# Performance work log

Measured on AMD Instinct MI355X. Metric: run time of the kernel, lower is better.

The kernel has to match this reference:

```python
import jax, jax.numpy as jnp
import numpy as np

EMBED_DIM = 768
FF_MULT = 4
HIDDEN = EMBED_DIM * FF_MULT
BATCH, SEQ = 32, 1024
EPS = 1e-6


def rmsnorm(x, g):
    # RMSNorm over last dim with learned scale g
    return x * jax.lax.rsqrt(jnp.mean(x * x, axis=-1, keepdims=True) + EPS) * g


def act_quant(x):
    # per-token int8 absmax quantization (BitNet b1.58)
    scale = 127.0 / jnp.clip(jnp.max(jnp.abs(x), axis=-1, keepdims=True), 1e-5, None)
    return jnp.clip(jnp.round(x * scale), -128.0, 127.0) / scale


def weight_quant(w):
    # per-tensor ternary (1.58-bit) absmean quantization
    scale = 1.0 / jnp.clip(jnp.mean(jnp.abs(w)), 1e-5, None)
    return jnp.clip(jnp.round(w * scale), -1.0, 1.0) / scale


def bitlinear(x, w, g):
    xn = rmsnorm(x, g)
    # straight-through estimator: forward uses quantized values
    xq = xn + jax.lax.stop_gradient(act_quant(xn) - xn)
    wq = w + jax.lax.stop_gradient(weight_quant(w) - w)
    return jnp.einsum('bsd,fd->bsf', xq, wq)


def setup_inputs() -> dict:
    key = jax.random.key(0)
    k1, k2, k3 = jax.random.split(key, 3)
    x = jax.random.normal(k1, (BATCH, SEQ, EMBED_DIM), dtype=jnp.float32)
    w1 = jax.random.normal(k2, (HIDDEN, EMBED_DIM), dtype=jnp.float32) * 0.02
    w2 = jax.random.normal(k3, (EMBED_DIM, HIDDEN), dtype=jnp.float32) * 0.02
    g1 = jnp.ones((EMBED_DIM,), dtype=jnp.float32)
    g2 = jnp.ones((HIDDEN,), dtype=jnp.float32)
    return {"x": x, "w1": w1, "g1": g1, "w2": w2, "g2": g2}


def reference(x, w1, g1, w2, g2):
    # BitFeedForward: BitLinear -> GELU (exact, matches nn.GELU) -> BitLinear
    # Dropout(p=0.0) is identity.
    h = jax.nn.gelu(bitlinear(x, w1, g1), approximate=False)
    return bitlinear(h, w2, g2)
```

## Files before the change

### kernel.cpp

```cpp
#include <hip/hip_runtime.h>
#include <hip/hip_bf16.h>
#include <hip/hip_fp16.h>
#include <math.h>

#define TOKENS 32768
#define EMBED  768
#define HIDDEN 3072
#define WELEMS (EMBED*HIDDEN)

typedef __attribute__((ext_vector_type(4))) int i32x4;
typedef signed char i8;

__device__ __forceinline__ float wave_reduce_sum(float v) {
    for (int o = 32; o > 0; o >>= 1) v += __shfl_down(v, o);
    return v;
}
__device__ __forceinline__ float wave_reduce_max(float v) {
    for (int o = 32; o > 0; o >>= 1) v = fmaxf(v, __shfl_down(v, o));
    return v;
}

__device__ __forceinline__ float gelu_tanh(float x) {
    const float x2 = x * x;
    const float u  = 0.7978845608f * x * fmaf(0.044715f, x2, 1.0f);
    const float ex = __expf(u + u);
    const float r  = __builtin_amdgcn_rcpf(ex + 1.0f);
    const float th = fmaf(-2.0f, r, 1.0f);
    const float hx = 0.5f * x;
    return fmaf(hx, th, hx);
}

__device__ __forceinline__ unsigned int q8pack4(float v0, float v1, float v2,
                                                float v3, float qs) {
    union { float f; unsigned int i; } u0, u1, u2, u3;
    u0.f = fmaf(v0, qs, 12582912.0f);
    u1.f = fmaf(v1, qs, 12582912.0f);
    u2.f = fmaf(v2, qs, 12582912.0f);
    u3.f = fmaf(v3, qs, 12582912.0f);
    return (u0.i & 0xFFu) | ((u1.i & 0xFFu) << 8) |
           ((u2.i & 0xFFu) << 16) | ((u3.i & 0xFFu) << 24);
}

__global__ __launch_bounds__(256) void k_abs_partial(const float* __restrict__ w,
                                                     float* __restrict__ out, int n) {
    float s = 0.f;
    for (int i = blockIdx.x * 256 + threadIdx.x; i < n; i += gridDim.x * 256)
        s += fabsf(w[i]);
    __shared__ float red[4];
    s = wave_reduce_sum(s);
    if ((threadIdx.x & 63) == 0) red[threadIdx.x >> 6] = s;
    __syncthreads();
    if (threadIdx.x == 0) out[blockIdx.x] = red[0] + red[1] + red[2] + red[3];
}

__global__ __launch_bounds__(256) void k_finalize(const float* __restrict__ p,
                                                  float* __restrict__ m) {
    __shared__ float r1[4], r2[4];
    float s1 = 0.f, s2 = 0.f;
    for (int i = threadIdx.x; i < 512; i += 256) { s1 += p[i]; s2 += p[512 + i]; }
    s1 = wave_reduce_sum(s1); s2 = wave_reduce_sum(s2);
    if ((threadIdx.x & 63) == 0) { r1[threadIdx.x >> 6] = s1; r2[threadIdx.x >> 6] = s2; }
    __syncthreads();
    if (threadIdx.x == 0) {
        float m1 = (r1[0] + r1[1] + r1[2] + r1[3]) / (float)WELEMS;
        float m2 = (r2[0] + r2[1] + r2[2] + r2[3]) / (float)WELEMS;
        m[0] = fmaxf(m1, 1e-5f);
        m[1] = fmaxf(m2, 1e-5f);
    }
}

__global__ __launch_bounds__(256) void k_quant_w(const float* __restrict__ w,
                                                 i8* __restrict__ wq,
                                                 const float* __restrict__ mp, int n) {
    const float inv = 1.0f / mp[0];
    for (int i = blockIdx.x * 256 + threadIdx.x; i < n; i += gridDim.x * 256) {
        float q = rintf(w[i] * inv);
        q = fminf(1.f, fmaxf(-1.f, q));
        wq[i] = (i8)(int)q;
    }
}

template <int D>
__global__ __launch_bounds__(256) void k_rms_quant_f32(const float* __restrict__ x,
                                                       const float* __restrict__ g,
                                                       i8* __restrict__ xq,
                                                       float* __restrict__ sc) {
    constexpr int NV = D / 4;
    constexpr int IT = (NV + 255) / 256;
    __shared__ float reds[4], redm[4];
    const int t = blockIdx.x;
    const float4* xp = reinterpret_cast<const float4*>(x + (size_t)t * D);
    const float4* gp = reinterpret_cast<const float4*>(g);
    float4 xg[IT];
    float ssq = 0.f, amax = 0.f;
#pragma unroll
    for (int i = 0; i < IT; ++i) {
        const int idx = i * 256 + (int)threadIdx.x;
        const bool act = (NV % 256 == 0) || (idx < NV);
        if (act) {
            float4 v = xp[idx];
            float4 gv = gp[idx];
            ssq += v.x * v.x + v.y * v.y + v.z * v.z + v.w * v.w;
            xg[i].x = v.x * gv.x; xg[i].y = v.y * gv.y;
            xg[i].z = v.z * gv.z; xg[i].w = v.w * gv.w;
            amax = fmaxf(amax, fmaxf(fmaxf(fabsf(xg[i].x), fabsf(xg[i].y)),
                                     fmaxf(fabsf(xg[i].z), fabsf(xg[i].w))));
        } else {
            xg[i].x = xg[i].y = xg[i].z = xg[i].w = 0.f;
        }
    }
    ssq = wave_reduce_sum(ssq);
    amax = wave_reduce_max(amax);
    if ((threadIdx.x & 63) == 0) { reds[threadIdx.x >> 6] = ssq; redm[threadIdx.x >> 6] = amax; }
    __syncthreads();
    const float S = reds[0] + reds[1] + reds[2] + reds[3];
    const float A = fmaxf(fmaxf(redm[0], redm[1]), fmaxf(redm[2], redm[3]));
    const float rs = (float)(1.0 / sqrt((double)S / D + 1e-6));
    const float an = fmaxf(A * rs, 1e-5f);
    const float qs = rs * (127.0f / an);
    if (threadIdx.x == 0) sc[t] = an * (1.0f / 127.0f);
    unsigned int* op = reinterpret_cast<unsigned int*>(xq + (size_t)t * D);
#pragma unroll
    for (int i = 0; i < IT; ++i) {
        const int idx = i * 256 + (int)threadIdx.x;
        const bool act = (NV % 256 == 0) || (idx < NV);
        if (act)
            op[idx] = q8pack4(xg[i].x, xg[i].y, xg[i].z, xg[i].w, qs);
    }
}

template <int D>
__global__ __launch_bounds__(256) void k_rms_quant_f16(const __half* __restrict__ x,
                                                       const float* __restrict__ g,
                                                       i8* __restrict__ xq,
                                                       float* __restrict__ sc) {
    constexpr int NV = D / 8;
    constexpr int IT = (NV + 255) / 256;
    __shared__ float reds[4], redm[4];
    const int t = blockIdx.x;
    const int4* xp = reinterpret_cast<const int4*>(x + (size_t)t * D);
    const float4* gp = reinterpret_cast<const float4*>(g);
    float xg[IT][8];
    float ssq = 0.f, amax = 0.f;
#pragma unroll
    for (int i = 0; i < IT; ++i) {
        const int idx = i * 256 + (int)threadIdx.x;
        const bool act = (NV % 256 == 0) || (idx < NV);
        if (act) {
            int4 raw = xp[idx];
            const __half2* hp = reinterpret_cast<const __half2*>(&raw);
            float4 g0 = gp[idx * 2];
            float4 g1 = gp[idx * 2 + 1];
            float gv[8] = {g0.x, g0.y, g0.z, g0.w, g1.x, g1.y, g1.z, g1.w};
#pragma unroll
            for (int j = 0; j < 4; ++j) {
                float2 f = __half22float2(hp[j]);
                float a0 = f.x, a1 = f.y;
                ssq += a0 * a0 + a1 * a1;
                xg[i][j * 2]     = a0 * gv[j * 2];
                xg[i][j * 2 + 1] = a1 * gv[j * 2 + 1];
                amax = fmaxf(amax, fmaxf(fabsf(xg[i][j * 2]), fabsf(xg[i][j * 2 + 1])));
            }
        } else {
#pragma unroll
            for (int j = 0; j < 8; ++j) xg[i][j] = 0.f;
        }
    }
    ssq = wave_reduce_sum(ssq);
    amax = wave_reduce_max(amax);
    if ((threadIdx.x & 63) == 0) { reds[threadIdx.x >> 6] = ssq; redm[threadIdx.x >> 6] = amax; }
    __syncthreads();
    const float S = reds[0] + reds[1] + reds[2] + reds[3];
    const float A = fmaxf(fmaxf(redm[0], redm[1]), fmaxf(redm[2], redm[3]));
    const float rs = (float)(1.0 / sqrt((double)S / D + 1e-6));
    const float an = fmaxf(A * rs, 1e-5f);
    const float qs = rs * (127.0f / an);
    if (threadIdx.x == 0) sc[t] = an * (1.0f / 127.0f);
    unsigned int* op = reinterpret_cast<unsigned int*>(xq + (size_t)t * D);
#pragma unroll
    for (int i = 0; i < IT; ++i) {
        const int idx = i * 256 + (int)threadIdx.x;
        const bool act = (NV % 256 == 0) || (idx < NV);
        if (act) {
            op[idx * 2]     = q8pack4(xg[i][0], xg[i][1], xg[i][2], xg[i][3], qs);
            op[idx * 2 + 1] = q8pack4(xg[i][4], xg[i][5], xg[i][6], xg[i][7], qs);
        }
    }
}

template <int BN, bool GELU, typename OutT>
__global__ __launch_bounds__(512, 4)
void k_gemm_i8(const i8* __restrict__ A, const i8* __restrict__ B,
               OutT* __restrict__ C, const float* __restrict__ rsc,
               const float* __restrict__ msc, int nbx, int N, int K) {
    constexpr int NI = BN / 64;
    __shared__ i8 As[128 * 128];
    __shared__ i8 Bs[BN * 128];

    const int nwg = (int)gridDim.x;
    const int id  = (int)blockIdx.x;
    const int q = nwg >> 3, r = nwg & 7;
    const int xcd = id & 7, sub = id >> 3;
    const int swz = (xcd < r ? xcd * (q + 1) : r * (q + 1) + (xcd - r) * q) + sub;
    const int bx = swz % nbx;
    const int by = swz / nbx;

    const int tid  = (int)threadIdx.x;
    const int lane = tid & 63;
    const int wave = tid >> 6;
    const int wr = wave >> 2, wc = wave & 3;
    const size_t rowBase = (size_t)by * 128;
    const size_t colBase = (size_t)bx * BN;
    const float ms = msc[0];

    i32x4 acc[4][NI] = {};

    const int srow = tid >> 3;
    const int cc   = tid & 7;
    const int gcol = (cc ^ (srow & 7)) * 16;
    const i8* gA0 = A + (rowBase + srow) * (size_t)K + gcol;
    const i8* gB0 = B + (colBase + srow) * (size_t)K + gcol;
    const int lOff = srow * 128 + cc * 16;

    const int frow = lane & 15;
    const int fko  = (lane >> 4) * 16;
    const int rswz = (frow & 7) << 4;

    for (int k0 = 0; k0 < K; k0 += 128) {
#pragma unroll
        for (int r2 = 0; r2 < 2; ++r2)
            __builtin_amdgcn_global_load_lds(
                (const __attribute__((address_space(1))) void*)(gA0 + (size_t)r2 * 64 * K + k0),
                (__attribute__((address_space(3))) void*)(&As[lOff + r2 * 64 * 128]), 16, 0, 0);
#pragma unroll
        for (int r4 = 0; r4 < BN / 64; ++r4)
            __builtin_amdgcn_global_load_lds(
                (const __attribute__((address_space(1))) void*)(gB0 + (size_t)r4 * 64 * K + k0),
                (__attribute__((address_space(3))) void*)(&Bs[lOff + r4 * 64 * 128]), 16, 0, 0);
        __syncthreads();
#pragma unroll
        for (int ks = 0; ks < 2; ++ks) {
            i32x4 af[4], bv[NI];
#pragma unroll
            for (int mi = 0; mi < 4; ++mi)
                af[mi] = *(const i32x4*)(&As[(wr * 64 + mi * 16 + frow) * 128
                                             + ((ks * 64 + fko) ^ rswz)]);
#pragma unroll
            for (int ni = 0; ni < NI; ++ni)
                bv[ni] = *(const i32x4*)(&Bs[(wc * (BN / 4) + ni * 16 + frow) * 128
                                             + ((ks * 64 + fko) ^ rswz)]);
#pragma unroll
            for (int mi = 0; mi < 4; ++mi)
#pragma unroll
                for (int ni = 0; ni < NI; ++ni)
                    acc[mi][ni] = __builtin_amdgcn_mfma_i32_16x16x64_i8(
                        af[mi], bv[ni], acc[mi][ni], 0, 0, 0);
        }
        __syncthreads();
    }

    const int ccol = lane & 15;
    const int crg  = lane >> 4;
#pragma unroll
    for (int mi = 0; mi < 4; ++mi) {
#pragma unroll
        for (int i = 0; i < 4; ++i) {
            size_t row = rowBase + wr * 64 + mi * 16 + crg * 4 + i;
            float rscale = rsc[row] * ms;
#pragma unroll
            for (int ni = 0; ni < NI; ++ni) {
                size_t col = colBase + wc * (BN / 4) + ni * 16 + ccol;
                float v = (float)acc[mi][ni][i] * rscale;
                if (GELU) v = gelu_tanh(v);
                C[row * (size_t)N + col] = (OutT)v;
            }
        }
    }
}

extern "C" void kernel_launch(void* const* d_in, const int* in_sizes, int n_in,
                              void* d_out, int out_size, void* d_ws, size_t ws_size,
                              hipStream_t stream) {
    const float* x  = (const float*)d_in[0];
    const float* w1 = (const float*)d_in[1];
    const float* g1 = (const float*)d_in[2];
    const float* w2 = (const float*)d_in[3];
    const float* g2 = (const float*)d_in[4];
    float* out = (float*)d_out;

    char* ws = (char*)d_ws;
    float* partials = (float*)ws;
    float* mvals    = (float*)(ws + 4096);
    float* a        = (float*)(ws + 4352);
    float* b        = (float*)(ws + 135424);
    i8*    wq1      = (i8*)(ws + 266496);
    i8*    wq2      = (i8*)(ws + 2625792);
    const size_t FIXED = 4985088;
    char* chunkMem = ws + FIXED;

    const size_t PER_TOK = 768 + 6144 + 3072;
    size_t avail = (ws_size > FIXED) ? (ws_size - FIXED) : 0;
    long long ch = (long long)(avail / PER_TOK);
    ch &= ~255LL;
    if (ch < 256) ch = 256;
    if (ch > TOKENS) ch = TOKENS;
    const int CH = (int)ch;

    k_abs_partial<<<512, 256, 0, stream>>>(w1, partials, WELEMS);
    k_abs_partial<<<512, 256, 0, stream>>>(w2, partials + 512, WELEMS);
    k_finalize<<<1, 256, 0, stream>>>(partials, mvals);
    k_quant_w<<<2048, 256, 0, stream>>>(w1, wq1, mvals + 0, WELEMS);
    k_quant_w<<<2048, 256, 0, stream>>>(w2, wq2, mvals + 1, WELEMS);

    for (int base = 0; base < TOKENS; base += CH) {
        const int rows = (TOKENS - base < CH) ? (TOKENS - base) : CH;
        i8*     xqc = (i8*)chunkMem;
        __half* hc  = (__half*)(chunkMem + (size_t)CH * 768);
        i8*     hqc = (i8*)(chunkMem + (size_t)CH * 768 + (size_t)CH * 6144);

        const int nby  = rows / 128;
        const int nbx1 = HIDDEN / 256;
        const int nbx2 = EMBED / 128;

        k_rms_quant_f32<EMBED><<<rows, 256, 0, stream>>>(
            x + (size_t)base * EMBED, g1, xqc, a + base);
        k_gemm_i8<256, true, __half><<<nbx1 * nby, 512, 0, stream>>>(
            xqc, wq1, hc, a + base, mvals + 0, nbx1, HIDDEN, EMBED);
        k_rms_quant_f16<HIDDEN><<<rows, 256, 0, stream>>>(
            hc, g2, hqc, b + base);
        k_gemm_i8<128, false, float><<<nbx2 * nby, 512, 0, stream>>>(
            hqc, wq2, out + (size_t)base * EMBED, b + base, mvals + 1, nbx2, EMBED, HIDDEN);
    }
}
```

Measured before the change: 343.0 us.

## Double-buffer int8 GEMM LDS tiles with K=64 steps and prefetch overlap

```diff
diff --git a/kernel.cpp b/kernel.cpp
--- a/kernel.cpp
+++ b/kernel.cpp
@@ -194,8 +194,9 @@
                OutT* __restrict__ C, const float* __restrict__ rsc,
                const float* __restrict__ msc, int nbx, int N, int K) {
     constexpr int NI = BN / 64;
-    __shared__ i8 As[128 * 128];
-    __shared__ i8 Bs[BN * 128];
+    constexpr int NLOADS = 1 + BN / 128;
+    __shared__ i8 As[2][64 * 128];
+    __shared__ i8 Bs[2][(BN / 2) * 128];
 
     const int nwg = (int)gridDim.x;
     const int id  = (int)blockIdx.x;
@@ -215,49 +216,85 @@
 
     i32x4 acc[4][NI] = {};
 
-    const int srow = tid >> 3;
-    const int cc   = tid & 7;
-    const int gcol = (cc ^ (srow & 7)) * 16;
-    const i8* gA0 = A + (rowBase + srow) * (size_t)K + gcol;
-    const i8* gB0 = B + (colBase + srow) * (size_t)K + gcol;
-    const int lOff = srow * 128 + cc * 16;
+    const int tl   = tid >> 3;
+    const int lch  = (tid & 7) ^ (tl & 7);
+    const int rloc = tl * 2 + (lch >> 2);
+    const int coff = (lch & 3) * 16;
+    const i8* gA = A + (rowBase + rloc) * (size_t)K + coff;
+    const i8* gB = B + (colBase + rloc) * (size_t)K + coff;
 
     const int frow = lane & 15;
-    const int fko  = (lane >> 4) * 16;
-    const int rswz = (frow & 7) << 4;
-
-    for (int k0 = 0; k0 < K; k0 += 128) {
-#pragma unroll
-        for (int r2 = 0; r2 < 2; ++r2)
-            __builtin_amdgcn_global_load_lds(
-                (const __attribute__((address_space(1))) void*)(gA0 + (size_t)r2 * 64 * K + k0),
-                (__attribute__((address_space(3))) void*)(&As[lOff + r2 * 64 * 128]), 16, 0, 0);
-#pragma unroll
-        for (int r4 = 0; r4 < BN / 64; ++r4)
-            __builtin_amdgcn_global_load_lds(
-                (const __attribute__((address_space(1))) void*)(gB0 + (size_t)r4 * 64 * K + k0),
-                (__attribute__((address_space(3))) void*)(&Bs[lOff + r4 * 64 * 128]), 16, 0, 0);
-        __syncthreads();
-#pragma unroll
-        for (int ks = 0; ks < 2; ++ks) {
-            i32x4 af[4], bv[NI];
-#pragma unroll
-            for (int mi = 0; mi < 4; ++mi)
-                af[mi] = *(const i32x4*)(&As[(wr * 64 + mi * 16 + frow) * 128
-                                             + ((ks * 64 + fko) ^ rswz)]);
+    const int fc   = lane >> 4;
+    int aaddr[4], baddr[NI];
+#pragma unroll
+    for (int mi = 0; mi < 4; ++mi) {
+        const int row = wr * 64 + mi * 16 + frow;
+        const int line = row >> 1;
+        const int sc = (((row & 1) << 2) + fc) ^ (line & 7);
+        aaddr[mi] = line * 128 + sc * 16;
+    }
+#pragma unroll
+    for (int ni = 0; ni < NI; ++ni) {
+        const int row = wc * (BN / 4) + ni * 16 + frow;
+        const int line = row >> 1;
+        const int sc = (((row & 1) << 2) + fc) ^ (line & 7);
+        baddr[ni] = line * 128 + sc * 16;
+    }
+
+    const int nt = K >> 6;
+
+#define STG(kk, buf)                                                           \
+    {                                                                          \
+        const int _k0 = (kk) << 6;                                             \
+        __builtin_amdgcn_global_load_lds(                                      \
+            (const __attribute__((address_space(1))) void*)(gA + _k0),         \
+            (__attribute__((address_space(3))) void*)(&As[buf][tid * 16]),     \
+            16, 0, 0);                                                         \
+        _Pragma("unroll")                                                      \
+        for (int _j = 0; _j < BN / 128; ++_j)                                  \
+            __builtin_amdgcn_global_load_lds(                                  \
+                (const __attribute__((address_space(1))) void*)                \
+                    (gB + (size_t)_j * 128 * K + _k0),                         \
+                (__attribute__((address_space(3))) void*)                      \
+                    (&Bs[buf][_j * 8192 + tid * 16]),                          \
+                16, 0, 0);                                                     \
+    }
+
+    STG(0, 0);
+
+    for (int t = 0; t < nt; ++t) {
+        const int cur = t & 1;
+        if (t + 1 < nt) {
+            STG(t + 1, cur ^ 1);
+            if constexpr (NLOADS == 3)
+                asm volatile("s_waitcnt vmcnt(3)" ::: "memory");
+            else
+                asm volatile("s_waitcnt vmcnt(2)" ::: "memory");
+        } else {
+            asm volatile("s_waitcnt vmcnt(0)" ::: "memory");
+        }
+        __builtin_amdgcn_s_barrier();
+        __builtin_amdgcn_sched_barrier(0);
+        i32x4 af[4], bv[NI];
+#pragma unroll
+        for (int mi = 0; mi < 4; ++mi)
+            af[mi] = *(const i32x4*)(&As[cur][aaddr[mi]]);
+#pragma unroll
+        for (int ni = 0; ni < NI; ++ni)
+            bv[ni] = *(const i32x4*)(&Bs[cur][baddr[ni]]);
+        __builtin_amdgcn_s_setprio(1);
+#pragma unroll
+        for (int mi = 0; mi < 4; ++mi)
 #pragma unroll
             for (int ni = 0; ni < NI; ++ni)
-                bv[ni] = *(const i32x4*)(&Bs[(wc * (BN / 4) + ni * 16 + frow) * 128
-                                             + ((ks * 64 + fko) ^ rswz)]);
-#pragma unroll
-            for (int mi = 0; mi < 4; ++mi)
-#pragma unroll
-                for (int ni = 0; ni < NI; ++ni)
-                    acc[mi][ni] = __builtin_amdgcn_mfma_i32_16x16x64_i8(
-                        af[mi], bv[ni], acc[mi][ni], 0, 0, 0);
-        }
-        __syncthreads();
-    }
+                acc[mi][ni] = __builtin_amdgcn_mfma_i32_16x16x64_i8(
+                    af[mi], bv[ni], acc[mi][ni], 0, 0, 0);
+        __builtin_amdgcn_s_setprio(0);
+        __builtin_amdgcn_sched_barrier(0);
+        __builtin_amdgcn_s_barrier();
+        __builtin_amdgcn_sched_barrier(0);
+    }
+#undef STG
 
     const int ccol = lane & 15;
     const int crg  = lane >> 4;
```

Measured after the change: 353.9 us. 3.2% more time.
